# Optimization experiments

Measured on AMD Instinct MI355X. Metric: run time of the kernel, lower is better.

Reference implementation:

```python
import jax, jax.numpy as jnp
import numpy as np

MAX_POS = 1024  # config.max_position_embeddings
NUM_HEADS = 16
HEAD_DIM = 64


def setup_inputs() -> dict:
    key = jax.random.key(0)
    ks = jax.random.split(key, 4)
    B, S, H = 4, 1024, 1024
    return {
        "hidden_states": jax.random.normal(ks[0], (B, S, H), dtype=jnp.float32),
        "qkv_w": jax.random.normal(ks[1], (3 * H, H), dtype=jnp.float32) * 0.02,
        "qkv_b": jax.random.normal(ks[2], (3 * H,), dtype=jnp.float32) * 0.02,
        "dist_emb": jax.random.normal(ks[3], (2 * MAX_POS - 1, HEAD_DIM), dtype=jnp.float32) * 0.02,
        "ext_mask": jnp.zeros((B, 1, 1, S), dtype=jnp.float32),
    }


def reference(hidden_states, qkv_w, qkv_b, dist_emb, ext_mask):
    B, S, H = hidden_states.shape
    h, d = NUM_HEADS, HEAD_DIM
    # fused QKV projection (q|k|v concatenated on output dim)
    qkv = jnp.einsum('bsi,oi->bso', hidden_states, qkv_w) + qkv_b
    q, k, v = jnp.split(qkv, 3, axis=-1)
    to_heads = lambda x: x.reshape(B, S, h, d).transpose(0, 2, 1, 3)  # [B,h,S,d]
    q, k, v = to_heads(q), to_heads(k), to_heads(v)
    # raw attention scores [B,h,S,S]
    scores = jnp.einsum('bhld,bhrd->bhlr', q, k)
    # relative_key_query positional bias
    pos = jnp.arange(S)
    distance = pos[:, None] - pos[None, :]          # [S,S]
    pe = dist_emb[distance + MAX_POS - 1]           # [S,S,d]
    scores = scores + jnp.einsum('bhld,lrd->bhlr', q, pe) \
                    + jnp.einsum('bhrd,lrd->bhlr', k, pe)
    scores = scores / jnp.sqrt(jnp.asarray(d, scores.dtype))
    scores = scores + ext_mask
    probs = jax.nn.softmax(scores, axis=-1)
    ctx = jnp.einsum('bhlr,bhrd->bhld', probs, v)   # [B,h,S,d]
    return ctx.transpose(0, 2, 1, 3).reshape(B, S, h * d)
```

## Files before the change

### kernel.cpp

```cpp
#include <hip/hip_runtime.h>

#define SEQ 1024
#define NH  16

typedef __attribute__((ext_vector_type(8))) short short8;
typedef __attribute__((ext_vector_type(4))) float floatx4;
typedef __attribute__((ext_vector_type(4))) unsigned short ushortx4;

#define GLDS16(gp, lp) __builtin_amdgcn_global_load_lds( \
    (const __attribute__((address_space(1))) void*)(gp), \
    (__attribute__((address_space(3))) void*)(lp), 16, 0, 0)

__device__ __forceinline__ unsigned short f2b(float f) {
    union { float f; unsigned u; } v; v.f = f;
    unsigned r = (v.u + 0x7fffu + ((v.u >> 16) & 1u)) >> 16;
    return (unsigned short)r;
}
__device__ __forceinline__ float b2f(unsigned short h) {
    union { unsigned u; float f; } v; v.u = ((unsigned)h) << 16;
    return v.f;
}

#define TADDR(base, row, ch) ((base) + ((row) << 6) + ((((ch) ^ ((row) & 7))) << 3))

__global__ void cast_kernel(const float* __restrict__ hs, const float* __restrict__ W,
                            const float* __restrict__ E,
                            unsigned short* __restrict__ hsb,
                            unsigned short* __restrict__ Wb,
                            unsigned short* __restrict__ Eb)
{
    const int QH = 1048576, QW = 786432, QE = 32752;
    const int NT = QH + QW + QE;
    for (int q = blockIdx.x * 256 + threadIdx.x; q < NT; q += gridDim.x * 256) {
        const float* src; unsigned short* dst; int off;
        if (q < QH)           { src = hs; dst = hsb; off = q; }
        else if (q < QH + QW) { src = W;  dst = Wb;  off = q - QH; }
        else                  { src = E;  dst = Eb;  off = q - QH - QW; }
        const float4 v = *(const float4*)(src + (size_t)off * 4);
        ushortx4 o; o[0] = f2b(v.x); o[1] = f2b(v.y); o[2] = f2b(v.z); o[3] = f2b(v.w);
        *(ushortx4*)(dst + (size_t)off * 4) = o;
    }
}

__global__ __launch_bounds__(256, 3) void qkv_gemm(
    const unsigned short* __restrict__ Ab, const unsigned short* __restrict__ Bb,
    const float* __restrict__ bias,
    unsigned short* __restrict__ Qb, unsigned short* __restrict__ Kb,
    unsigned short* __restrict__ Vt)
{
    __shared__ unsigned short sm[8192];
    const int t = threadIdx.x, w = t >> 6;
    const int ln = t & 15, g = (t >> 4) & 3;
    const int wm = w >> 1, wn = w & 1;
    const int m0 = blockIdx.y << 7, o0 = blockIdx.x << 7;

    floatx4 acc[4][4];
#pragma unroll
    for (int i = 0; i < 4; ++i)
#pragma unroll
        for (int j = 0; j < 4; ++j) acc[i][j] = (floatx4){0.f, 0.f, 0.f, 0.f};

    auto stage = [&](int kb) {
#pragma unroll
        for (int p = 0; p < 2; ++p) {
            const int idx = (p << 8) + t;
            const int row = idx >> 2;
            const int c = (idx & 3) ^ ((row ^ (row >> 2)) & 3);
            GLDS16(Ab + (size_t)(m0 + row) * 1024 + kb + (c << 3),
                   (char*)sm + (p << 12) + (w << 10));
            GLDS16(Bb + (size_t)(o0 + row) * 1024 + kb + (c << 3),
                   (char*)sm + 8192 + (p << 12) + (w << 10));
        }
    };

    stage(0);
    for (int kb = 0;;) {
        __syncthreads();
        short8 af[4], bf_[4];
#pragma unroll
        for (int i = 0; i < 4; ++i) {
            const int r = (wm << 6) + (i << 4) + ln;
            af[i] = *(const short8*)&sm[(r << 5) + ((g ^ ((r ^ (r >> 2)) & 3)) << 3)];
        }
#pragma unroll
        for (int j = 0; j < 4; ++j) {
            const int r = (wn << 6) + (j << 4) + ln;
            bf_[j] = *(const short8*)&sm[4096 + (r << 5) + ((g ^ ((r ^ (r >> 2)) & 3)) << 3)];
        }
#pragma unroll
        for (int i = 0; i < 4; ++i)
#pragma unroll
            for (int j = 0; j < 4; ++j)
                acc[i][j] = __builtin_amdgcn_mfma_f32_16x16x32_bf16(af[i], bf_[j], acc[i][j], 0, 0, 0);
        kb += 32;
        if (kb >= 1024) break;
        __syncthreads();
        stage(kb);
    }

    const int which = o0 >> 10;
    float bj[4];
#pragma unroll
    for (int j = 0; j < 4; ++j) bj[j] = bias[o0 + (wn << 6) + (j << 4) + ln];

    if (which == 2) {
#pragma unroll
        for (int i = 0; i < 4; ++i) {
            const int m = m0 + (wm << 6) + (i << 4) + (g << 2);
            const int b = m >> 10, s = m & 1023;
#pragma unroll
            for (int j = 0; j < 4; ++j) {
                const int o = o0 + (wn << 6) + (j << 4) + ln;
                const int d = o & 63, hh = (o >> 6) & 15;
                ushortx4 pk;
#pragma unroll
                for (int q = 0; q < 4; ++q) pk[q] = f2b(acc[i][j][q] + bj[j]);
                *(ushortx4*)(Vt + (((size_t)((b << 4) + hh)) << 16) + (d << 10) + s) = pk;
            }
        }
    } else {
        unsigned short* dst = which ? Kb : Qb;
        const float sc = which ? 1.0f : 0.125f;
#pragma unroll
        for (int i = 0; i < 4; ++i)
#pragma unroll
            for (int q = 0; q < 4; ++q) {
                const int m = m0 + (wm << 6) + (i << 4) + (g << 2) + q;
                const int b = m >> 10, s = m & 1023;
#pragma unroll
                for (int j = 0; j < 4; ++j) {
                    const int o = o0 + (wn << 6) + (j << 4) + ln;
                    const int d = o & 63, hh = (o >> 6) & 15;
                    dst[(((size_t)((b << 4) + hh)) << 16) + (s << 6) + d] =
                        f2b((acc[i][j][q] + bj[j]) * sc);
                }
            }
    }
}

__global__ __launch_bounds__(256, 3) void attn_mfma(
    const unsigned short* __restrict__ Qb, const unsigned short* __restrict__ Kb,
    const unsigned short* __restrict__ Vt, const unsigned short* __restrict__ Eb,
    const float* __restrict__ mask, float* __restrict__ outp)
{
    __shared__ __align__(16) unsigned short sm[25600];
    const int t = threadIdx.x, w = t >> 6;
    const int wu = __builtin_amdgcn_readfirstlane(w);
    const int ln = t & 15, g = (t >> 4) & 3;
    const int bid = blockIdx.x;
    const int swz = ((bid & 7) << 7) | (bid >> 3);
    const int bh = swz >> 4;
    const int l0 = (swz & 15) << 6;
    const int b = bh >> 4, h = bh & 15;
    const size_t hb = (size_t)bh << 16;
    const int x0 = (w << 4) + (g << 2);

    const int qr = (w << 4) + ln;
    const short8 qa0 = *(const short8*)(Qb + hb + ((size_t)(l0 + qr) << 6) + (g << 3));
    const short8 qa1 = *(const short8*)(Qb + hb + ((size_t)(l0 + qr) << 6) + 32 + (g << 3));

    floatx4 O[4];
    float mr[4], lr[4];
#pragma unroll
    for (int dt = 0; dt < 4; ++dt) O[dt] = (floatx4){0.f, 0.f, 0.f, 0.f};
#pragma unroll
    for (int q = 0; q < 4; ++q) { mr[q] = -1e30f; lr[q] = 0.f; }

    for (int r0 = 0; r0 < SEQ; r0 += 64) {
        __syncthreads();
#pragma unroll
        for (int p = 0; p < 2; ++p) {
            const int idx = (p << 8) + t;
            const int row = idx >> 3;
            const int c = (idx & 7) ^ (row & 7);
            GLDS16(Kb + hb + ((size_t)(r0 + row) << 6) + (c << 3),
                   (char*)sm + (p << 12) + (w << 10));
        }
        const int j0 = l0 - r0 + 960;
#pragma unroll
        for (int p = 0; p < 4; ++p) {
            const int idx = (p << 8) + t;
            const int row = idx >> 3;
            const int c = (idx & 7) ^ (row & 7);
            GLDS16(Eb + ((size_t)(j0 + row) << 6) + (c << 3),
                   (char*)sm + 8192 + (p << 12) + (w << 10));
        }
        __syncthreads();
        short8 kf[4][2];
#pragma unroll
        for (int j = 0; j < 4; ++j) {
            const int kr = (j << 4) + ln;
            kf[j][0] = *(const short8*)&sm[TADDR(0, kr, g)];
            kf[j][1] = *(const short8*)&sm[TADDR(0, kr, 4 + g)];
        }
        const int wr = (w << 4) + ln;
        const short8 ka0 = *(const short8*)&sm[TADDR(0, wr, g)];
        const short8 ka1 = *(const short8*)&sm[TADDR(0, wr, 4 + g)];

        floatx4 S[4];
#pragma unroll
        for (int j = 0; j < 4; ++j) {
            floatx4 z = (floatx4){0.f, 0.f, 0.f, 0.f};
            z = __builtin_amdgcn_mfma_f32_16x16x32_bf16(qa0, kf[j][0], z, 0, 0, 0);
            S[j] = __builtin_amdgcn_mfma_f32_16x16x32_bf16(qa1, kf[j][1], z, 0, 0, 0);
        }
#pragma unroll
        for (int dt = 0; dt < 8; ++dt) {
            const bool doU = (dt >= wu) && (dt <= wu + 4);
            const bool doW = (dt >= 3 - wu) && (dt <= 7 - wu);
            if (!doU && !doW) continue;
            const int er = (dt << 4) + ln;
            const short8 e0 = *(const short8*)&sm[TADDR(4096, er, g)];
            const short8 e1 = *(const short8*)&sm[TADDR(4096, er, 4 + g)];
            if (doU) {
                floatx4 z = (floatx4){0.f, 0.f, 0.f, 0.f};
                z = __builtin_amdgcn_mfma_f32_16x16x32_bf16(qa0, e0, z, 0, 0, 0);
                const floatx4 U = __builtin_amdgcn_mfma_f32_16x16x32_bf16(qa1, e1, z, 0, 0, 0);
                int a = 12288 + (x0 - (dt << 4) - ln + 79) * 72 + x0;
#pragma unroll
                for (int q = 0; q < 4; ++q) { sm[a] = f2b(U[q]); a += 73; }
            }
            if (doW) {
                floatx4 z2 = (floatx4){0.f, 0.f, 0.f, 0.f};
                z2 = __builtin_amdgcn_mfma_f32_16x16x32_bf16(ka0, e0, z2, 0, 0, 0);
                const floatx4 Wv = __builtin_amdgcn_mfma_f32_16x16x32_bf16(ka1, e1, z2, 0, 0, 0);
                int a = 19200 + x0 * 101 + (dt << 4) + ln - 47;
#pragma unroll
                for (int q = 0; q < 4; ++q) { sm[a] = f2b(Wv[q] * 0.125f); a += 101; }
            }
        }
        __syncthreads();
#pragma unroll
        for (int p = 0; p < 2; ++p) {
            const int idx = (p << 8) + t;
            const int row = idx >> 3;
            const int c = (idx & 7) ^ (row & 7);
            GLDS16(Vt + hb + ((size_t)row << 10) + r0 + (c << 3),
                   (char*)sm + 8192 + (p << 12) + (w << 10));
        }
        float Pw[4][4];
#pragma unroll
        for (int j = 0; j < 4; ++j) {
            const int rr = (j << 4) + ln;
            const float mk = mask[(b << 10) + r0 + rr];
            const ushortx4 u4 = *(const ushortx4*)&sm[12288 + (rr + 16) * 72 + x0];
            const ushortx4 w4 = *(const ushortx4*)&sm[19200 + rr * 100 + 16 + x0];
#pragma unroll
            for (int q = 0; q < 4; ++q)
                S[j][q] += b2f(u4[q]) + b2f(w4[q]) + mk;
        }
#pragma unroll
        for (int q = 0; q < 4; ++q) {
            float tm = fmaxf(fmaxf(S[0][q], S[1][q]), fmaxf(S[2][q], S[3][q]));
            tm = fmaxf(tm, __shfl_xor(tm, 1));
            tm = fmaxf(tm, __shfl_xor(tm, 2));
            tm = fmaxf(tm, __shfl_xor(tm, 4));
            tm = fmaxf(tm, __shfl_xor(tm, 8));
            const float mnew = fmaxf(mr[q], tm);
            const float al = __expf(mr[q] - mnew);
            float sum = 0.f;
#pragma unroll
            for (int j = 0; j < 4; ++j) {
                const float p = __expf(S[j][q] - mnew);
                Pw[j][q] = p; sum += p;
            }
            sum += __shfl_xor(sum, 1);
            sum += __shfl_xor(sum, 2);
            sum += __shfl_xor(sum, 4);
            sum += __shfl_xor(sum, 8);
            lr[q] = lr[q] * al + sum;
            mr[q] = mnew;
#pragma unroll
            for (int dt = 0; dt < 4; ++dt) O[dt][q] *= al;
        }
#pragma unroll
        for (int j = 0; j < 4; ++j) {
            const int rr = (j << 4) + ln;
#pragma unroll
            for (int q = 0; q < 4; ++q) {
                const int l = x0 + q;
                sm[8192 + (l << 6) + ((((rr >> 3) ^ (l & 7)) << 3)) + (rr & 7)] = f2b(Pw[j][q]);
            }
        }
        __syncthreads();
        const int pr = (w << 4) + ln;
        const short8 pa0 = *(const short8*)&sm[TADDR(8192, pr, g)];
        const short8 pa1 = *(const short8*)&sm[TADDR(8192, pr, 4 + g)];
#pragma unroll
        for (int dt = 0; dt < 4; ++dt) {
            const int vr = (dt << 4) + ln;
            const short8 v0 = *(const short8*)&sm[TADDR(4096, vr, g)];
            const short8 v1 = *(const short8*)&sm[TADDR(4096, vr, 4 + g)];
            O[dt] = __builtin_amdgcn_mfma_f32_16x16x32_bf16(pa0, v0, O[dt], 0, 0, 0);
            O[dt] = __builtin_amdgcn_mfma_f32_16x16x32_bf16(pa1, v1, O[dt], 0, 0, 0);
        }
    }
#pragma unroll
    for (int dt = 0; dt < 4; ++dt)
#pragma unroll
        for (int q = 0; q < 4; ++q) {
            const int l = x0 + q;
            outp[((size_t)b << 20) + ((size_t)(l0 + l) << 10) + (h << 6) + (dt << 4) + ln]
                = O[dt][q] / lr[q];
        }
}

extern "C" void kernel_launch(void* const* d_in, const int* in_sizes, int n_in,
                              void* d_out, int out_size, void* d_ws, size_t ws_size,
                              hipStream_t stream)
{
    const float* hs   = (const float*)d_in[0];
    const float* qkvw = (const float*)d_in[1];
    const float* qkvb = (const float*)d_in[2];
    const float* demb = (const float*)d_in[3];
    const float* mask = (const float*)d_in[4];
    float* out = (float*)d_out;

    char* ws = (char*)d_ws;
    unsigned short* hsb = (unsigned short*)(ws);
    unsigned short* Wb  = (unsigned short*)(ws + 8388608);
    unsigned short* Eb  = (unsigned short*)(ws + 14680064);
    unsigned short* Qb  = (unsigned short*)(ws + 14942208);
    unsigned short* Kb  = (unsigned short*)(ws + 23330816);
    unsigned short* Vt  = (unsigned short*)(ws + 31719424);

    cast_kernel<<<2048, 256, 0, stream>>>(hs, qkvw, demb, hsb, Wb, Eb);
    qkv_gemm<<<dim3(24, 32), 256, 0, stream>>>(hsb, Wb, qkvb, Qb, Kb, Vt);
    attn_mfma<<<1024, 256, 0, stream>>>(Qb, Kb, Vt, Eb, mask, out);
}
```

Measured before the change: 230.2 us.

## Double-buffer V tiles and read K/E fragments directly from global memory

Stops staging the K and distance-embedding tiles through LDS; each lane now loads its MFMA fragments straight from global memory, which removes one barrier per iteration. V tiles are double-buffered in LDS and the next tile is prefetched during softmax, so its transfer overlaps compute. The LDS layout is remapped: two V buffers, then the U/W bias regions, then P. The trade-off is redundant, less coalesced global reads of K and E across waves, relying on the cache.

```diff
diff --git a/kernel.cpp b/kernel.cpp
--- a/kernel.cpp
+++ b/kernel.cpp
@@ -159,43 +159,42 @@
     const short8 qa0 = *(const short8*)(Qb + hb + ((size_t)(l0 + qr) << 6) + (g << 3));
     const short8 qa1 = *(const short8*)(Qb + hb + ((size_t)(l0 + qr) << 6) + 32 + (g << 3));
 
-    floatx4 O[4];
-    float mr[4], lr[4];
-#pragma unroll
-    for (int dt = 0; dt < 4; ++dt) O[dt] = (floatx4){0.f, 0.f, 0.f, 0.f};
-#pragma unroll
-    for (int q = 0; q < 4; ++q) { mr[q] = -1e30f; lr[q] = 0.f; }
-
-    for (int r0 = 0; r0 < SEQ; r0 += 64) {
-        __syncthreads();
+    auto stageV = [&](int rb, int buf) {
 #pragma unroll
         for (int p = 0; p < 2; ++p) {
             const int idx = (p << 8) + t;
             const int row = idx >> 3;
             const int c = (idx & 7) ^ (row & 7);
-            GLDS16(Kb + hb + ((size_t)(r0 + row) << 6) + (c << 3),
-                   (char*)sm + (p << 12) + (w << 10));
-        }
+            GLDS16(Vt + hb + ((size_t)row << 10) + rb + (c << 3),
+                   (char*)sm + (buf << 13) + (p << 12) + (w << 10));
+        }
+    };
+
+    stageV(0, 0);
+
+    floatx4 O[4];
+    float mr[4], lr[4];
+#pragma unroll
+    for (int dt = 0; dt < 4; ++dt) O[dt] = (floatx4){0.f, 0.f, 0.f, 0.f};
+#pragma unroll
+    for (int q = 0; q < 4; ++q) { mr[q] = -1e30f; lr[q] = 0.f; }
+
+    __syncthreads();
+
+    for (int r0 = 0; r0 < SEQ; r0 += 64) {
         const int j0 = l0 - r0 + 960;
-#pragma unroll
-        for (int p = 0; p < 4; ++p) {
-            const int idx = (p << 8) + t;
-            const int row = idx >> 3;
-            const int c = (idx & 7) ^ (row & 7);
-            GLDS16(Eb + ((size_t)(j0 + row) << 6) + (c << 3),
-                   (char*)sm + 8192 + (p << 12) + (w << 10));
-        }
-        __syncthreads();
+        const int vb = (r0 >> 6) & 1;
+
         short8 kf[4][2];
 #pragma unroll
         for (int j = 0; j < 4; ++j) {
-            const int kr = (j << 4) + ln;
-            kf[j][0] = *(const short8*)&sm[TADDR(0, kr, g)];
-            kf[j][1] = *(const short8*)&sm[TADDR(0, kr, 4 + g)];
-        }
-        const int wr = (w << 4) + ln;
-        const short8 ka0 = *(const short8*)&sm[TADDR(0, wr, g)];
-        const short8 ka1 = *(const short8*)&sm[TADDR(0, wr, 4 + g)];
+            const size_t kro = hb + ((size_t)(r0 + (j << 4) + ln) << 6);
+            kf[j][0] = *(const short8*)(Kb + kro + (g << 3));
+            kf[j][1] = *(const short8*)(Kb + kro + 32 + (g << 3));
+        }
+        const size_t kwo = hb + ((size_t)(r0 + (w << 4) + ln) << 6);
+        const short8 ka0 = *(const short8*)(Kb + kwo + (g << 3));
+        const short8 ka1 = *(const short8*)(Kb + kwo + 32 + (g << 3));
 
         floatx4 S[4];
 #pragma unroll
@@ -209,14 +208,14 @@
             const bool doU = (dt >= wu) && (dt <= wu + 4);
             const bool doW = (dt >= 3 - wu) && (dt <= 7 - wu);
             if (!doU && !doW) continue;
-            const int er = (dt << 4) + ln;
-            const short8 e0 = *(const short8*)&sm[TADDR(4096, er, g)];
-            const short8 e1 = *(const short8*)&sm[TADDR(4096, er, 4 + g)];
+            const size_t ero = (size_t)(j0 + (dt << 4) + ln) << 6;
+            const short8 e0 = *(const short8*)(Eb + ero + (g << 3));
+            const short8 e1 = *(const short8*)(Eb + ero + 32 + (g << 3));
             if (doU) {
                 floatx4 z = (floatx4){0.f, 0.f, 0.f, 0.f};
                 z = __builtin_amdgcn_mfma_f32_16x16x32_bf16(qa0, e0, z, 0, 0, 0);
                 const floatx4 U = __builtin_amdgcn_mfma_f32_16x16x32_bf16(qa1, e1, z, 0, 0, 0);
-                int a = 12288 + (x0 - (dt << 4) - ln + 79) * 72 + x0;
+                int a = 8192 + (x0 - (dt << 4) - ln + 79) * 72 + x0;
 #pragma unroll
                 for (int q = 0; q < 4; ++q) { sm[a] = f2b(U[q]); a += 73; }
             }
@@ -224,27 +223,22 @@
                 floatx4 z2 = (floatx4){0.f, 0.f, 0.f, 0.f};
                 z2 = __builtin_amdgcn_mfma_f32_16x16x32_bf16(ka0, e0, z2, 0, 0, 0);
                 const floatx4 Wv = __builtin_amdgcn_mfma_f32_16x16x32_bf16(ka1, e1, z2, 0, 0, 0);
-                int a = 19200 + x0 * 101 + (dt << 4) + ln - 47;
+                int a = 15104 + x0 * 101 + (dt << 4) + ln - 47;
 #pragma unroll
                 for (int q = 0; q < 4; ++q) { sm[a] = f2b(Wv[q] * 0.125f); a += 101; }
             }
         }
         __syncthreads();
-#pragma unroll
-        for (int p = 0; p < 2; ++p) {
-            const int idx = (p << 8) + t;
-            const int row = idx >> 3;
-            const int c = (idx & 7) ^ (row & 7);
-            GLDS16(Vt + hb + ((size_t)row << 10) + r0 + (c << 3),
-                   (char*)sm + 8192 + (p << 12) + (w << 10));
-        }
+
+        if (r0 < 960) stageV(r0 + 64, vb ^ 1);
+
         float Pw[4][4];
 #pragma unroll
         for (int j = 0; j < 4; ++j) {
             const int rr = (j << 4) + ln;
             const float mk = mask[(b << 10) + r0 + rr];
-            const ushortx4 u4 = *(const ushortx4*)&sm[12288 + (rr + 16) * 72 + x0];
-            const ushortx4 w4 = *(const ushortx4*)&sm[19200 + rr * 100 + 16 + x0];
+            const ushortx4 u4 = *(const ushortx4*)&sm[8192 + (rr + 16) * 72 + x0];
+            const ushortx4 w4 = *(const ushortx4*)&sm[15104 + rr * 100 + 16 + x0];
 #pragma unroll
             for (int q = 0; q < 4; ++q)
                 S[j][q] += b2f(u4[q]) + b2f(w4[q]) + mk;
@@ -279,18 +273,20 @@
 #pragma unroll
             for (int q = 0; q < 4; ++q) {
                 const int l = x0 + q;
-                sm[8192 + (l << 6) + ((((rr >> 3) ^ (l & 7)) << 3)) + (rr & 7)] = f2b(Pw[j][q]);
+                sm[21504 + (l << 6) + ((((rr >> 3) ^ (l & 7)) << 3)) + (rr & 7)] = f2b(Pw[j][q]);
             }
         }
         __syncthreads();
+
         const int pr = (w << 4) + ln;
-        const short8 pa0 = *(const short8*)&sm[TADDR(8192, pr, g)];
-        const short8 pa1 = *(const short8*)&sm[TADDR(8192, pr, 4 + g)];
+        const short8 pa0 = *(const short8*)&sm[TADDR(21504, pr, g)];
+        const short8 pa1 = *(const short8*)&sm[TADDR(21504, pr, 4 + g)];
+        const int vbase = vb << 12;
 #pragma unroll
         for (int dt = 0; dt < 4; ++dt) {
             const int vr = (dt << 4) + ln;
-            const short8 v0 = *(const short8*)&sm[TADDR(4096, vr, g)];
-            const short8 v1 = *(const short8*)&sm[TADDR(4096, vr, 4 + g)];
+            const short8 v0 = *(const short8*)&sm[TADDR(vbase, vr, g)];
+            const short8 v1 = *(const short8*)&sm[TADDR(vbase, vr, 4 + g)];
             O[dt] = __builtin_amdgcn_mfma_f32_16x16x32_bf16(pa0, v0, O[dt], 0, 0, 0);
             O[dt] = __builtin_amdgcn_mfma_f32_16x16x32_bf16(pa1, v1, O[dt], 0, 0, 0);
         }
```

Result: slower. 414.2 us (+80.0%).

## Prefetch next K/E/V tiles with double-buffered V and ring-buffered E

Applied to the files above, without the earlier changes.

Restructures the attention loop so the next iteration's K, the new 64 rows of the distance-embedding window, and the next V tile are issued as async global-to-LDS loads mid-iteration. V is double-buffered, and E is kept as a 128-row ring indexed by XOR, so only 64 new rows are fetched per step instead of 128. This removes the load-then-barrier stall at the top of each iteration and halves E traffic. The cost is a larger LDS footprint (about 74KB) and lowering launch bounds from 3 to 2 blocks per CU, which reduces occupancy.

```diff
diff --git a/kernel.cpp b/kernel.cpp
--- a/kernel.cpp
+++ b/kernel.cpp
@@ -138,12 +138,12 @@
     }
 }
 
-__global__ __launch_bounds__(256, 3) void attn_mfma(
+__global__ __launch_bounds__(256, 2) void attn_mfma(
     const unsigned short* __restrict__ Qb, const unsigned short* __restrict__ Kb,
     const unsigned short* __restrict__ Vt, const unsigned short* __restrict__ Eb,
     const float* __restrict__ mask, float* __restrict__ outp)
 {
-    __shared__ __align__(16) unsigned short sm[25600];
+    __shared__ __align__(16) unsigned short sm[37888];
     const int t = threadIdx.x, w = t >> 6;
     const int wu = __builtin_amdgcn_readfirstlane(w);
     const int ln = t & 15, g = (t >> 4) & 3;
@@ -159,6 +159,53 @@
     const short8 qa0 = *(const short8*)(Qb + hb + ((size_t)(l0 + qr) << 6) + (g << 3));
     const short8 qa1 = *(const short8*)(Qb + hb + ((size_t)(l0 + qr) << 6) + 32 + (g << 3));
 
+    auto stageK = [&](int rb) {
+#pragma unroll
+        for (int p = 0; p < 2; ++p) {
+            const int idx = (p << 8) + t;
+            const int row = idx >> 3;
+            const int c = (idx & 7) ^ (row & 7);
+            GLDS16(Kb + hb + ((size_t)(rb + row) << 6) + (c << 3),
+                   (char*)sm + (p << 12) + (w << 10));
+        }
+    };
+    auto stageV = [&](int rb, int buf) {
+#pragma unroll
+        for (int p = 0; p < 2; ++p) {
+            const int idx = (p << 8) + t;
+            const int row = idx >> 3;
+            const int c = (idx & 7) ^ (row & 7);
+            GLDS16(Vt + hb + ((size_t)row << 10) + rb + (c << 3),
+                   (char*)sm + 8192 + (buf << 13) + (p << 12) + (w << 10));
+        }
+    };
+    auto stageE64 = [&](int j0n) {
+        const int ejn = j0n & 64;
+#pragma unroll
+        for (int p = 0; p < 2; ++p) {
+            const int idx = (p << 8) + t;
+            const int row = idx >> 3;
+            const int c = (idx & 7) ^ (row & 7);
+            GLDS16(Eb + ((size_t)(j0n + row) << 6) + (c << 3),
+                   (char*)sm + 24576 + (ejn << 7) + (p << 12) + (w << 10));
+        }
+    };
+
+    stageK(0);
+    {
+        const int j0p = l0 + 960, ejp = j0p & 64;
+#pragma unroll
+        for (int p = 0; p < 4; ++p) {
+            const int idx = (p << 8) + t;
+            const int prow = idx >> 3;
+            const int arow = j0p + (prow ^ ejp);
+            const int c = (idx & 7) ^ (prow & 7);
+            GLDS16(Eb + ((size_t)arow << 6) + (c << 3),
+                   (char*)sm + 24576 + (p << 12) + (w << 10));
+        }
+    }
+    stageV(0, 0);
+
     floatx4 O[4];
     float mr[4], lr[4];
 #pragma unroll
@@ -166,26 +213,13 @@
 #pragma unroll
     for (int q = 0; q < 4; ++q) { mr[q] = -1e30f; lr[q] = 0.f; }
 
+    __syncthreads();
+
     for (int r0 = 0; r0 < SEQ; r0 += 64) {
-        __syncthreads();
-#pragma unroll
-        for (int p = 0; p < 2; ++p) {
-            const int idx = (p << 8) + t;
-            const int row = idx >> 3;
-            const int c = (idx & 7) ^ (row & 7);
-            GLDS16(Kb + hb + ((size_t)(r0 + row) << 6) + (c << 3),
-                   (char*)sm + (p << 12) + (w << 10));
-        }
         const int j0 = l0 - r0 + 960;
-#pragma unroll
-        for (int p = 0; p < 4; ++p) {
-            const int idx = (p << 8) + t;
-            const int row = idx >> 3;
-            const int c = (idx & 7) ^ (row & 7);
-            GLDS16(Eb + ((size_t)(j0 + row) << 6) + (c << 3),
-                   (char*)sm + 8192 + (p << 12) + (w << 10));
-        }
-        __syncthreads();
+        const int ej = j0 & 64;
+        const int vb = (r0 >> 6) & 1;
+
         short8 kf[4][2];
 #pragma unroll
         for (int j = 0; j < 4; ++j) {
@@ -209,14 +243,14 @@
             const bool doU = (dt >= wu) && (dt <= wu + 4);
             const bool doW = (dt >= 3 - wu) && (dt <= 7 - wu);
             if (!doU && !doW) continue;
-            const int er = (dt << 4) + ln;
-            const short8 e0 = *(const short8*)&sm[TADDR(4096, er, g)];
-            const short8 e1 = *(const short8*)&sm[TADDR(4096, er, 4 + g)];
+            const int ephys = ((dt << 4) + ln) ^ ej;
+            const short8 e0 = *(const short8*)&sm[TADDR(12288, ephys, g)];
+            const short8 e1 = *(const short8*)&sm[TADDR(12288, ephys, 4 + g)];
             if (doU) {
                 floatx4 z = (floatx4){0.f, 0.f, 0.f, 0.f};
                 z = __builtin_amdgcn_mfma_f32_16x16x32_bf16(qa0, e0, z, 0, 0, 0);
                 const floatx4 U = __builtin_amdgcn_mfma_f32_16x16x32_bf16(qa1, e1, z, 0, 0, 0);
-                int a = 12288 + (x0 - (dt << 4) - ln + 79) * 72 + x0;
+                int a = 20480 + (x0 - (dt << 4) - ln + 79) * 72 + x0;
 #pragma unroll
                 for (int q = 0; q < 4; ++q) { sm[a] = f2b(U[q]); a += 73; }
             }
@@ -224,27 +258,26 @@
                 floatx4 z2 = (floatx4){0.f, 0.f, 0.f, 0.f};
                 z2 = __builtin_amdgcn_mfma_f32_16x16x32_bf16(ka0, e0, z2, 0, 0, 0);
                 const floatx4 Wv = __builtin_amdgcn_mfma_f32_16x16x32_bf16(ka1, e1, z2, 0, 0, 0);
-                int a = 19200 + x0 * 101 + (dt << 4) + ln - 47;
+                int a = 27392 + x0 * 101 + (dt << 4) + ln - 47;
 #pragma unroll
                 for (int q = 0; q < 4; ++q) { sm[a] = f2b(Wv[q] * 0.125f); a += 101; }
             }
         }
         __syncthreads();
-#pragma unroll
-        for (int p = 0; p < 2; ++p) {
-            const int idx = (p << 8) + t;
-            const int row = idx >> 3;
-            const int c = (idx & 7) ^ (row & 7);
-            GLDS16(Vt + hb + ((size_t)row << 10) + r0 + (c << 3),
-                   (char*)sm + 8192 + (p << 12) + (w << 10));
-        }
+
+        if (r0 < 960) {
+            stageK(r0 + 64);
+            stageE64(j0 - 64);
+            stageV(r0 + 64, vb ^ 1);
+        }
+
         float Pw[4][4];
 #pragma unroll
         for (int j = 0; j < 4; ++j) {
             const int rr = (j << 4) + ln;
             const float mk = mask[(b << 10) + r0 + rr];
-            const ushortx4 u4 = *(const ushortx4*)&sm[12288 + (rr + 16) * 72 + x0];
-            const ushortx4 w4 = *(const ushortx4*)&sm[19200 + rr * 100 + 16 + x0];
+            const ushortx4 u4 = *(const ushortx4*)&sm[20480 + (rr + 16) * 72 + x0];
+            const ushortx4 w4 = *(const ushortx4*)&sm[27392 + rr * 100 + 16 + x0];
 #pragma unroll
             for (int q = 0; q < 4; ++q)
                 S[j][q] += b2f(u4[q]) + b2f(w4[q]) + mk;
@@ -279,18 +312,20 @@
 #pragma unroll
             for (int q = 0; q < 4; ++q) {
                 const int l = x0 + q;
-                sm[8192 + (l << 6) + ((((rr >> 3) ^ (l & 7)) << 3)) + (rr & 7)] = f2b(Pw[j][q]);
+                sm[33792 + (l << 6) + ((((rr >> 3) ^ (l & 7)) << 3)) + (rr & 7)] = f2b(Pw[j][q]);
             }
         }
         __syncthreads();
+
         const int pr = (w << 4) + ln;
-        const short8 pa0 = *(const short8*)&sm[TADDR(8192, pr, g)];
-        const short8 pa1 = *(const short8*)&sm[TADDR(8192, pr, 4 + g)];
+        const short8 pa0 = *(const short8*)&sm[TADDR(33792, pr, g)];
+        const short8 pa1 = *(const short8*)&sm[TADDR(33792, pr, 4 + g)];
+        const int vbase = 4096 + (vb << 12);
 #pragma unroll
         for (int dt = 0; dt < 4; ++dt) {
             const int vr = (dt << 4) + ln;
-            const short8 v0 = *(const short8*)&sm[TADDR(4096, vr, g)];
-            const short8 v1 = *(const short8*)&sm[TADDR(4096, vr, 4 + g)];
+            const short8 v0 = *(const short8*)&sm[TADDR(vbase, vr, g)];
+            const short8 v1 = *(const short8*)&sm[TADDR(vbase, vr, 4 + g)];
             O[dt] = __builtin_amdgcn_mfma_f32_16x16x32_bf16(pa0, v0, O[dt], 0, 0, 0);
             O[dt] = __builtin_amdgcn_mfma_f32_16x16x32_bf16(pa1, v1, O[dt], 0, 0, 0);
         }
```

Result: no change. 228.4 us (-0.8%).

## Accumulate relative-position bias via fp32 LDS atomics and raise occupancy to four blocks

Applied to the files above, without the earlier changes.

The attention kernel now adds both relative-position bias terms with fp32 LDS atomicAdd into one swizzled 64x64 buffer. Previously each term was written as bf16 into its own padded skewed staging area. This frees LDS (51KB down to 40KB), so launch bounds go from 3 to 4 blocks per CU, and the P tile now reuses the K region. It also adds s_setprio around the MFMA sections and hoists the mask loads to the top of each iteration. LDS atomics cost more than plain stores and the higher occupancy limits registers per thread, but keeping the bias in fp32 avoids bf16 rounding.

```diff
diff --git a/kernel.cpp b/kernel.cpp
--- a/kernel.cpp
+++ b/kernel.cpp
@@ -138,12 +138,13 @@
     }
 }
 
-__global__ __launch_bounds__(256, 3) void attn_mfma(
+__global__ __launch_bounds__(256, 4) void attn_mfma(
     const unsigned short* __restrict__ Qb, const unsigned short* __restrict__ Kb,
     const unsigned short* __restrict__ Vt, const unsigned short* __restrict__ Eb,
     const float* __restrict__ mask, float* __restrict__ outp)
 {
-    __shared__ __align__(16) unsigned short sm[25600];
+    __shared__ __align__(16) unsigned short sm[20480];
+    float* uwf = (float*)&sm[12288];
     const int t = threadIdx.x, w = t >> 6;
     const int wu = __builtin_amdgcn_readfirstlane(w);
     const int ln = t & 15, g = (t >> 4) & 3;
@@ -154,11 +155,18 @@
     const int b = bh >> 4, h = bh & 15;
     const size_t hb = (size_t)bh << 16;
     const int x0 = (w << 4) + (g << 2);
+    const int cb = x0 >> 2;
 
     const int qr = (w << 4) + ln;
     const short8 qa0 = *(const short8*)(Qb + hb + ((size_t)(l0 + qr) << 6) + (g << 3));
     const short8 qa1 = *(const short8*)(Qb + hb + ((size_t)(l0 + qr) << 6) + 32 + (g << 3));
 
+#pragma unroll
+    for (int j = 0; j < 4; ++j) {
+        const int rr = (j << 4) + ln;
+        *(floatx4*)&uwf[(rr << 6) + ((cb ^ (rr & 15)) << 2)] = (floatx4){0.f, 0.f, 0.f, 0.f};
+    }
+
     floatx4 O[4];
     float mr[4], lr[4];
 #pragma unroll
@@ -167,6 +175,10 @@
     for (int q = 0; q < 4; ++q) { mr[q] = -1e30f; lr[q] = 0.f; }
 
     for (int r0 = 0; r0 < SEQ; r0 += 64) {
+        float mk4[4];
+#pragma unroll
+        for (int j = 0; j < 4; ++j) mk4[j] = mask[(b << 10) + r0 + (j << 4) + ln];
+
         __syncthreads();
 #pragma unroll
         for (int p = 0; p < 2; ++p) {
@@ -186,6 +198,7 @@
                    (char*)sm + 8192 + (p << 12) + (w << 10));
         }
         __syncthreads();
+
         short8 kf[4][2];
 #pragma unroll
         for (int j = 0; j < 4; ++j) {
@@ -197,6 +210,7 @@
         const short8 ka0 = *(const short8*)&sm[TADDR(0, wr, g)];
         const short8 ka1 = *(const short8*)&sm[TADDR(0, wr, 4 + g)];
 
+        __builtin_amdgcn_s_setprio(1);
         floatx4 S[4];
 #pragma unroll
         for (int j = 0; j < 4; ++j) {
@@ -216,20 +230,30 @@
                 floatx4 z = (floatx4){0.f, 0.f, 0.f, 0.f};
                 z = __builtin_amdgcn_mfma_f32_16x16x32_bf16(qa0, e0, z, 0, 0, 0);
                 const floatx4 U = __builtin_amdgcn_mfma_f32_16x16x32_bf16(qa1, e1, z, 0, 0, 0);
-                int a = 12288 + (x0 - (dt << 4) - ln + 79) * 72 + x0;
-#pragma unroll
-                for (int q = 0; q < 4; ++q) { sm[a] = f2b(U[q]); a += 73; }
+#pragma unroll
+                for (int q = 0; q < 4; ++q) {
+                    const int ru = x0 + q - (dt << 4) - ln + 63;
+                    if ((unsigned)ru < 64u)
+                        atomicAdd(&uwf[(ru << 6) + (((cb ^ (ru & 15)) << 2) | q)], U[q]);
+                }
             }
             if (doW) {
                 floatx4 z2 = (floatx4){0.f, 0.f, 0.f, 0.f};
                 z2 = __builtin_amdgcn_mfma_f32_16x16x32_bf16(ka0, e0, z2, 0, 0, 0);
                 const floatx4 Wv = __builtin_amdgcn_mfma_f32_16x16x32_bf16(ka1, e1, z2, 0, 0, 0);
-                int a = 19200 + x0 * 101 + (dt << 4) + ln - 47;
-#pragma unroll
-                for (int q = 0; q < 4; ++q) { sm[a] = f2b(Wv[q] * 0.125f); a += 101; }
-            }
-        }
-        __syncthreads();
+#pragma unroll
+                for (int q = 0; q < 4; ++q) {
+                    const int lw = x0 + q + (dt << 4) + ln - 63;
+                    if ((unsigned)lw < 64u)
+                        atomicAdd(&uwf[((x0 + q) << 6) +
+                                       ((((lw >> 2) ^ ((x0 + q) & 15)) << 2) | (lw & 3))],
+                                  Wv[q] * 0.125f);
+                }
+            }
+        }
+        __builtin_amdgcn_s_setprio(0);
+        __syncthreads();
+
 #pragma unroll
         for (int p = 0; p < 2; ++p) {
             const int idx = (p << 8) + t;
@@ -242,12 +266,12 @@
 #pragma unroll
         for (int j = 0; j < 4; ++j) {
             const int rr = (j << 4) + ln;
-            const float mk = mask[(b << 10) + r0 + rr];
-            const ushortx4 u4 = *(const ushortx4*)&sm[12288 + (rr + 16) * 72 + x0];
-            const ushortx4 w4 = *(const ushortx4*)&sm[19200 + rr * 100 + 16 + x0];
+            float* pc = &uwf[(rr << 6) + ((cb ^ (rr & 15)) << 2)];
+            const floatx4 s4 = *(const floatx4*)pc;
+            *(floatx4*)pc = (floatx4){0.f, 0.f, 0.f, 0.f};
 #pragma unroll
             for (int q = 0; q < 4; ++q)
-                S[j][q] += b2f(u4[q]) + b2f(w4[q]) + mk;
+                S[j][q] += s4[q] + mk4[j];
         }
 #pragma unroll
         for (int q = 0; q < 4; ++q) {
@@ -279,13 +303,15 @@
 #pragma unroll
             for (int q = 0; q < 4; ++q) {
                 const int l = x0 + q;
-                sm[8192 + (l << 6) + ((((rr >> 3) ^ (l & 7)) << 3)) + (rr & 7)] = f2b(Pw[j][q]);
-            }
-        }
-        __syncthreads();
+                sm[(l << 6) + ((((rr >> 3) ^ (l & 7)) << 3)) + (rr & 7)] = f2b(Pw[j][q]);
+            }
+        }
+        __syncthreads();
+
         const int pr = (w << 4) + ln;
-        const short8 pa0 = *(const short8*)&sm[TADDR(8192, pr, g)];
-        const short8 pa1 = *(const short8*)&sm[TADDR(8192, pr, 4 + g)];
+        const short8 pa0 = *(const short8*)&sm[TADDR(0, pr, g)];
+        const short8 pa1 = *(const short8*)&sm[TADDR(0, pr, 4 + g)];
+        __builtin_amdgcn_s_setprio(1);
 #pragma unroll
         for (int dt = 0; dt < 4; ++dt) {
             const int vr = (dt << 4) + ln;
@@ -294,6 +320,7 @@
             O[dt] = __builtin_amdgcn_mfma_f32_16x16x32_bf16(pa0, v0, O[dt], 0, 0, 0);
             O[dt] = __builtin_amdgcn_mfma_f32_16x16x32_bf16(pa1, v1, O[dt], 0, 0, 0);
         }
+        __builtin_amdgcn_s_setprio(0);
     }
 #pragma unroll
     for (int dt = 0; dt < 4; ++dt)
```

After: 875.3 us. +280.3%, slower.
